# Kernel tuning notes

Hardware: AMD Instinct MI355X
Metric: run time of the kernel (lower is better)

The kernel has to match this reference:

```python
import jax, jax.numpy as jnp
import numpy as np

NX, NY = 2, 4          # Cpab tess_size [2, 4]
NT = 4 * NX * NY       # 4 triangles per cell = 32
NSTEPS = 50            # libcpab default numeric integration steps


def _build_tess():
    corner, verts = {}, []
    for j in range(NY + 1):
        for i in range(NX + 1):
            corner[(i, j)] = len(verts); verts.append((i / NX, j / NY))
    center = {}
    for j in range(NY):
        for i in range(NX):
            center[(i, j)] = len(verts); verts.append(((i + 0.5) / NX, (j + 0.5) / NY))
    verts = np.array(verts, np.float64)
    # zero_boundary=True: only interior grid corners + cell centers carry free velocity
    free = [corner[(i, j)] for j in range(1, NY) for i in range(1, NX)]
    free += [center[(i, j)] for j in range(NY) for i in range(NX)]
    tri_vidx = np.zeros((NT, 3), np.int32)
    invP = np.zeros((NT, 3, 3), np.float64)
    for j in range(NY):
        for i in range(NX):
            ll, lr = corner[(i, j)], corner[(i + 1, j)]
            ur, ul = corner[(i + 1, j + 1)], corner[(i, j + 1)]
            c = center[(i, j)]
            for k, tv in enumerate([(ll, lr, c), (lr, ur, c), (ur, ul, c), (ul, ll, c)]):
                t = 4 * (i + j * NX) + k
                tri_vidx[t] = tv
                P = np.vstack([verts[list(tv)].T, np.ones(3)])  # columns [p; 1]
                invP[t] = np.linalg.inv(P)
    return np.array(free, np.int32), tri_vidx, invP.astype(np.float32), len(verts)

FREE_IDX, TRI_VIDX, INVP, NV = _build_tess()
THETA_DIM = 2 * len(FREE_IDX)  # 22


def _findcell(p):
    # p: (..., 2) in [0,1]^2 -> flat triangle index in [0, NT)
    x = jnp.clip(p[..., 0], 0.0, 1.0) * NX
    y = jnp.clip(p[..., 1], 0.0, 1.0) * NY
    cx = jnp.clip(jnp.floor(x), 0, NX - 1)
    cy = jnp.clip(jnp.floor(y), 0, NY - 1)
    xr, yr = x - cx, y - cy
    below_diag = yr <= xr
    below_anti = yr <= 1.0 - xr
    tri = jnp.where(below_diag, jnp.where(below_anti, 0, 1),
                    jnp.where(below_anti, 3, 2))
    return (4 * (cx + cy * NX)).astype(jnp.int32) + tri


def _cpab_transform_grid(theta, H, W):
    # theta (B, 22) -> per-triangle affine maps A (B, NT, 2, 3), then Euler-integrate
    B = theta.shape[0]
    vv = jnp.zeros((B, NV, 2), theta.dtype).at[:, FREE_IDX].set(theta.reshape(B, -1, 2))
    V = vv[:, TRI_VIDX]                                            # (B,NT,3,2) vertex velocities
    A = jnp.einsum('btvc,tvw->btcw', V, jnp.asarray(INVP, theta.dtype))  # (B,NT,2,3)
    gx, gy = jnp.meshgrid(jnp.linspace(0.0, 1.0, W), jnp.linspace(0.0, 1.0, H))
    p0 = jnp.broadcast_to(jnp.stack([gx.ravel(), gy.ravel()], -1), (B, H * W, 2))
    dt = 1.0 / NSTEPS
    bidx = jnp.arange(B)[:, None]

    def step(p, _):
        Ai = A[bidx, _findcell(p)]                                 # (B,HW,2,3)
        v = Ai[..., 0] * p[..., :1] + Ai[..., 1] * p[..., 1:2] + Ai[..., 2]
        return p + dt * v, None

    p, _ = jax.lax.scan(step, p0, None, length=NSTEPS)
    return p                                                       # (B,HW,2)


def _bilinear(data, grid, H, W):
    # data (B,C,H,W), grid (B,HW,2) in [0,1]; clamp-to-border bilinear sampling
    B, C = data.shape[0], data.shape[1]
    gx = jnp.clip(grid[..., 0], 0.0, 1.0) * (W - 1)
    gy = jnp.clip(grid[..., 1], 0.0, 1.0) * (H - 1)
    x0 = jnp.clip(jnp.floor(gx).astype(jnp.int32), 0, W - 2)
    y0 = jnp.clip(jnp.floor(gy).astype(jnp.int32), 0, H - 2)
    wx, wy = gx - x0, gy - y0
    df = data.reshape(B, C, H * W)
    take = jax.vmap(lambda d, l: d[:, l])                          # per-batch gather

    def g(ix, iy):
        return take(df, iy * W + ix)                               # (B,C,HW)

    wx_, wy_ = wx[:, None, :], wy[:, None, :]
    out = (g(x0, y0) * (1 - wx_) * (1 - wy_)
           + g(x0 + 1, y0) * wx_ * (1 - wy_)
           + g(x0, y0 + 1) * (1 - wx_) * wy_
           + g(x0 + 1, y0 + 1) * wx_ * wy_)
    return out.reshape(B, C, H, W)


def setup_inputs() -> dict:
    key = jax.random.key(0)
    k1, k2 = jax.random.split(key)
    x = jax.random.normal(k1, (8, 256, 256, 64), dtype=jnp.float32)
    theta = jax.random.normal(k2, (8, THETA_DIM), dtype=jnp.float32)
    return {"x": x, "theta": theta}


def reference(x, theta):
    B, H, W, C = x.shape
    data = jnp.transpose(x, (0, 3, 1, 2))          # NHWC -> NCHW
    grid_t = _cpab_transform_grid(theta, H, W)     # integrate CPA velocity field
    out = _bilinear(data, grid_t, H, W)            # warp via bilinear sampling
    return jnp.transpose(out, (0, 2, 3, 1))        # NCHW -> NHWC
```

## Files before the change

### kernel.cpp

```cpp
#include <hip/hip_runtime.h>

#define NBATCH 8
#define HH 256
#define WW 256
#define CC 64
#define HWPTS 65536
#define NSTEPS_ 50

typedef float vf4 __attribute__((ext_vector_type(4)));

__global__ __launch_bounds__(256) void cpab_build_A(const float* __restrict__ theta,
                                                    float* __restrict__ Aout) {
  int tid = threadIdx.x;
  int b = tid >> 5, t = tid & 31;
  int cell = t >> 2, k = t & 3;
  int ci = cell & 1, cj = cell >> 1;
  int ll = cj * 3 + ci;
  int lr = ll + 1, ul = ll + 3, ur = ll + 4;
  int cen = 15 + cj * 2 + ci;
  int v0, v1, v2 = cen;
  if (k == 0)      { v0 = ll; v1 = lr; }
  else if (k == 1) { v0 = lr; v1 = ur; }
  else if (k == 2) { v0 = ur; v1 = ul; }
  else             { v0 = ul; v1 = ll; }

  int vs[3] = {v0, v1, v2};
  double xs[3], ys[3];
  float Vx[3], Vy[3];
  for (int q = 0; q < 3; ++q) {
    int v = vs[q];
    if (v < 15) { xs[q] = (double)(v % 3) * 0.5; ys[q] = (double)(v / 3) * 0.25; }
    else { int u = v - 15; xs[q] = ((double)(u & 1) + 0.5) * 0.5;
           ys[q] = ((double)(u >> 1) + 0.5) * 0.25; }
    int s = (v == 4) ? 0 : (v == 7) ? 1 : (v == 10) ? 2 : (v >= 15) ? (v - 12) : -1;
    if (s >= 0) { Vx[q] = theta[b * 22 + 2 * s]; Vy[q] = theta[b * 22 + 2 * s + 1]; }
    else        { Vx[q] = 0.f; Vy[q] = 0.f; }
  }
  double x0 = xs[0], x1 = xs[1], x2 = xs[2];
  double y0 = ys[0], y1 = ys[1], y2 = ys[2];
  double det = x0 * (y1 - y2) - x1 * (y0 - y2) + x2 * (y0 - y1);
  double inv[3][3] = {
      {y1 - y2, x2 - x1, x1 * y2 - x2 * y1},
      {y2 - y0, x0 - x2, x2 * y0 - x0 * y2},
      {y0 - y1, x1 - x0, x0 * y1 - x1 * y0}};
  for (int w = 0; w < 3; ++w) {
    float i0 = (float)(inv[0][w] / det);
    float i1 = (float)(inv[1][w] / det);
    float i2 = (float)(inv[2][w] / det);
    float ax = __fadd_rn(__fadd_rn(__fmul_rn(Vx[0], i0), __fmul_rn(Vx[1], i1)),
                         __fmul_rn(Vx[2], i2));
    float ay = __fadd_rn(__fadd_rn(__fmul_rn(Vy[0], i0), __fmul_rn(Vy[1], i1)),
                         __fmul_rn(Vy[2], i2));
    Aout[b * 192 + (w * 32 + t) * 2]     = ax;
    Aout[b * 192 + (w * 32 + t) * 2 + 1] = ay;
  }
}

__global__ __launch_bounds__(256) void cpab_warp_sample(const float* __restrict__ xin,
                                                        const float* __restrict__ Ain,
                                                        float* __restrict__ out) {
  __shared__ float2 sA2[96];
  __shared__ int    sOff[256];
  __shared__ float4 sW[256];

  int tid = threadIdx.x;
  int bid = blockIdx.x;
  int swz = ((bid & 7) << 8) | (bid >> 3);
  int base_pt = swz << 8;
  int b = bid & 7;

  if (tid < 192) ((float*)sA2)[tid] = Ain[b * 192 + tid];
  __syncthreads();

  {
    int hw = (base_pt + tid) & (HWPTS - 1);
    int w = hw & 255, h = hw >> 8;
    float px = (w == 255) ? 1.0f : __fmul_rn((float)w, 1.0f / 255.0f);
    float py = (h == 255) ? 1.0f : __fmul_rn((float)h, 1.0f / 255.0f);
#pragma unroll 1
    for (int s = 0; s < NSTEPS_; ++s) {
      float xc = fminf(fmaxf(px, 0.f), 1.f) * 2.0f;
      float yc = fminf(fmaxf(py, 0.f), 1.f) * 4.0f;
      float cxf = fminf(floorf(xc), 1.0f);
      float cyf = fminf(floorf(yc), 3.0f);
      float xr = xc - cxf, yr = yc - cyf;
      int tri = (yr <= xr) ? ((yr <= 1.0f - xr) ? 0 : 1)
                           : ((yr <= 1.0f - xr) ? 3 : 2);
      int cid = ((((int)cyf) << 1) + (int)cxf) * 4 + tri;
      float2 q0 = sA2[cid];
      float2 q1 = sA2[32 + cid];
      float2 q2 = sA2[64 + cid];
      float vx = __fadd_rn(__fadd_rn(__fmul_rn(q0.x, px), __fmul_rn(q1.x, py)), q2.x);
      float vy = __fadd_rn(__fadd_rn(__fmul_rn(q0.y, px), __fmul_rn(q1.y, py)), q2.y);
      px = __fadd_rn(px, __fmul_rn(0.02f, vx));
      py = __fadd_rn(py, __fmul_rn(0.02f, vy));
    }
    float gx = __fmul_rn(fminf(fmaxf(px, 0.f), 1.f), 255.0f);
    float gy = __fmul_rn(fminf(fmaxf(py, 0.f), 1.f), 255.0f);
    int ix = min((int)gx, 254);
    int iy = min((int)gy, 254);
    float wx = __fadd_rn(gx, -(float)ix);
    float wy = __fadd_rn(gy, -(float)iy);
    sOff[tid] = (iy << 8) + ix;
    float4 w4;
    w4.x = (1.f - wx) * (1.f - wy);
    w4.y = wx * (1.f - wy);
    w4.z = (1.f - wx) * wy;
    w4.w = wx * wy;
    sW[tid] = w4;
  }
  __syncthreads();

  const float4* xb4 = (const float4*)(xin + (size_t)b * ((size_t)HWPTS * CC));
  float* ob = out + (size_t)base_pt * CC;
  int lane_c = tid & 15;
  int lane_p = tid >> 4;

#pragma unroll
  for (int r = 0; r < 4; ++r) {
    float4 L[4][4];
    float4 W[4];
    const float4* q[4];
#pragma unroll
    for (int g = 0; g < 4; ++g) {
      int p = r * 16 + lane_p + g * 64;
      int off = sOff[p];
      W[g] = sW[p];
      q[g] = xb4 + ((size_t)off << 4) + lane_c;
    }
#pragma unroll
    for (int g = 0; g < 4; ++g) {
      L[g][0] = q[g][0];
      L[g][1] = q[g][16];
      L[g][2] = q[g][16 * 256];
      L[g][3] = q[g][16 * 256 + 16];
    }
#pragma unroll
    for (int g = 0; g < 4; ++g) {
      int p = r * 16 + lane_p + g * 64;
      vf4 o;
      o.x = L[g][0].x * W[g].x + L[g][1].x * W[g].y + L[g][2].x * W[g].z + L[g][3].x * W[g].w;
      o.y = L[g][0].y * W[g].x + L[g][1].y * W[g].y + L[g][2].y * W[g].z + L[g][3].y * W[g].w;
      o.z = L[g][0].z * W[g].x + L[g][1].z * W[g].y + L[g][2].z * W[g].z + L[g][3].z * W[g].w;
      o.w = L[g][0].w * W[g].x + L[g][1].w * W[g].y + L[g][2].w * W[g].z + L[g][3].w * W[g].w;
      __builtin_nontemporal_store(o, (vf4*)(ob + (size_t)p * CC + (lane_c << 2)));
    }
  }
}

extern "C" void kernel_launch(void* const* d_in, const int* in_sizes, int n_in,
                              void* d_out, int out_size, void* d_ws, size_t ws_size,
                              hipStream_t stream) {
  const float* x     = (const float*)d_in[0];
  const float* theta = (const float*)d_in[1];
  float* out  = (float*)d_out;
  float* Abuf = (float*)d_ws;

  cpab_build_A<<<1, 256, 0, stream>>>(theta, Abuf);
  cpab_warp_sample<<<NBATCH * HWPTS / 256, 256, 0, stream>>>(x, Abuf, out);
}
```

Measured before the change: 44.33 us.

## Make sampling phase wave-local, drop block barrier, remap blocks to rows

Each block now handles one full image row of one batch, so a wave samples only the 64 points its own threads integrated. That lets the second __syncthreads be removed. The sampling loop becomes a 16-iteration per-wave loop with one point per lane group, and launch bounds request 8 blocks per CU for occupancy. The change is meant to cut barrier stalls and register pressure. It relies on wave-local LDS visibility without a barrier, which holds only if a wave is exactly 64 lanes, and it drops the earlier block swizzle, which may alter cache locality.

```diff
diff --git a/kernel.cpp b/kernel.cpp
--- a/kernel.cpp
+++ b/kernel.cpp
@@ -56,27 +56,25 @@
   }
 }
 
-__global__ __launch_bounds__(256) void cpab_warp_sample(const float* __restrict__ xin,
-                                                        const float* __restrict__ Ain,
-                                                        float* __restrict__ out) {
+__global__ __launch_bounds__(256, 8) void cpab_warp_sample(const float* __restrict__ xin,
+                                                           const float* __restrict__ Ain,
+                                                           float* __restrict__ out) {
   __shared__ float2 sA2[96];
   __shared__ int    sOff[256];
   __shared__ float4 sW[256];
 
   int tid = threadIdx.x;
   int bid = blockIdx.x;
-  int swz = ((bid & 7) << 8) | (bid >> 3);
-  int base_pt = swz << 8;
   int b = bid & 7;
+  int row = bid >> 3;
+  int base_hw = row << 8;
 
   if (tid < 192) ((float*)sA2)[tid] = Ain[b * 192 + tid];
   __syncthreads();
 
   {
-    int hw = (base_pt + tid) & (HWPTS - 1);
-    int w = hw & 255, h = hw >> 8;
-    float px = (w == 255) ? 1.0f : __fmul_rn((float)w, 1.0f / 255.0f);
-    float py = (h == 255) ? 1.0f : __fmul_rn((float)h, 1.0f / 255.0f);
+    float px = (tid == 255) ? 1.0f : __fmul_rn((float)tid, 1.0f / 255.0f);
+    float py = (row == 255) ? 1.0f : __fmul_rn((float)row, 1.0f / 255.0f);
 #pragma unroll 1
     for (int s = 0; s < NSTEPS_; ++s) {
       float xc = fminf(fmaxf(px, 0.f), 1.f) * 2.0f;
@@ -109,42 +107,29 @@
     w4.w = wx * wy;
     sW[tid] = w4;
   }
-  __syncthreads();
 
+  int wv = tid >> 6;
+  int lp = (tid >> 4) & 3;
+  int lc = tid & 15;
   const float4* xb4 = (const float4*)(xin + (size_t)b * ((size_t)HWPTS * CC));
-  float* ob = out + (size_t)base_pt * CC;
-  int lane_c = tid & 15;
-  int lane_p = tid >> 4;
+  float* ob = out + ((size_t)b * HWPTS + base_hw + (wv << 6)) * CC;
 
 #pragma unroll
-  for (int r = 0; r < 4; ++r) {
-    float4 L[4][4];
-    float4 W[4];
-    const float4* q[4];
-#pragma unroll
-    for (int g = 0; g < 4; ++g) {
-      int p = r * 16 + lane_p + g * 64;
-      int off = sOff[p];
-      W[g] = sW[p];
-      q[g] = xb4 + ((size_t)off << 4) + lane_c;
-    }
-#pragma unroll
-    for (int g = 0; g < 4; ++g) {
-      L[g][0] = q[g][0];
-      L[g][1] = q[g][16];
-      L[g][2] = q[g][16 * 256];
-      L[g][3] = q[g][16 * 256 + 16];
-    }
-#pragma unroll
-    for (int g = 0; g < 4; ++g) {
-      int p = r * 16 + lane_p + g * 64;
-      vf4 o;
-      o.x = L[g][0].x * W[g].x + L[g][1].x * W[g].y + L[g][2].x * W[g].z + L[g][3].x * W[g].w;
-      o.y = L[g][0].y * W[g].x + L[g][1].y * W[g].y + L[g][2].y * W[g].z + L[g][3].y * W[g].w;
-      o.z = L[g][0].z * W[g].x + L[g][1].z * W[g].y + L[g][2].z * W[g].z + L[g][3].z * W[g].w;
-      o.w = L[g][0].w * W[g].x + L[g][1].w * W[g].y + L[g][2].w * W[g].z + L[g][3].w * W[g].w;
-      __builtin_nontemporal_store(o, (vf4*)(ob + (size_t)p * CC + (lane_c << 2)));
-    }
+  for (int i = 0; i < 16; ++i) {
+    int p = (wv << 6) + (i << 2) + lp;
+    int off = sOff[p];
+    float4 W = sW[p];
+    const float4* q = xb4 + ((size_t)off << 4) + lc;
+    float4 L0 = q[0];
+    float4 L1 = q[16];
+    float4 L2 = q[16 * 256];
+    float4 L3 = q[16 * 256 + 16];
+    vf4 o;
+    o.x = L0.x * W.x + L1.x * W.y + L2.x * W.z + L3.x * W.w;
+    o.y = L0.y * W.x + L1.y * W.y + L2.y * W.z + L3.y * W.w;
+    o.z = L0.z * W.x + L1.z * W.y + L2.z * W.z + L3.z * W.w;
+    o.w = L0.w * W.x + L1.w * W.y + L2.w * W.z + L3.w * W.w;
+    __builtin_nontemporal_store(o, (vf4*)(ob + (size_t)((i << 2) + lp) * CC + (lc << 2)));
   }
 }
 
```

Result: slower. 51.17 us (+15.5%).
